# Performance work log

Measured on AMD Instinct MI355X. Metric: run time of the kernel, lower is better.

The kernel has to match this reference:

```python
import jax, jax.numpy as jnp
import numpy as np

B, T, E, H = 2, 2048, 1024, 16
HS = E // H  # head size = 64
EPS = 1e-5


def setup_inputs() -> dict:
    key = jax.random.key(0)
    ks = jax.random.split(key, 12)
    s_e = 1.0 / np.sqrt(E)
    s_4e = 1.0 / np.sqrt(4 * E)
    return {
        "x": jax.random.normal(ks[0], (B, T, E), dtype=jnp.float32),
        # per-head projections (no bias), stacked over heads: [H, E, HS]
        "Wq": jax.random.uniform(ks[1], (H, E, HS), jnp.float32, -s_e, s_e),
        "Wk": jax.random.uniform(ks[2], (H, E, HS), jnp.float32, -s_e, s_e),
        "Wv": jax.random.uniform(ks[3], (H, E, HS), jnp.float32, -s_e, s_e),
        # output projection
        "Wo": jax.random.uniform(ks[4], (E, E), jnp.float32, -s_e, s_e),
        "bo": jax.random.uniform(ks[5], (E,), jnp.float32, -s_e, s_e),
        # feed-forward
        "W1": jax.random.uniform(ks[6], (E, 4 * E), jnp.float32, -s_e, s_e),
        "b1": jax.random.uniform(ks[7], (4 * E,), jnp.float32, -s_e, s_e),
        "W2": jax.random.uniform(ks[8], (4 * E, E), jnp.float32, -s_4e, s_4e),
        "b2": jax.random.uniform(ks[9], (E,), jnp.float32, -s_4e, s_4e),
        # layernorms
        "g1": jnp.ones((E,), jnp.float32),
        "be1": jnp.zeros((E,), jnp.float32),
        "g2": jnp.ones((E,), jnp.float32),
        "be2": jnp.zeros((E,), jnp.float32),
    }


def _layernorm(x, g, b):
    mu = jnp.mean(x, axis=-1, keepdims=True)
    var = jnp.var(x, axis=-1, keepdims=True)
    return (x - mu) * jax.lax.rsqrt(var + EPS) * g + b


def reference(x, Wq, Wk, Wv, Wo, bo, W1, b1, W2, b2, g1, be1, g2, be2):
    Bx, Tx, Ex = x.shape
    # --- multi-head causal self-attention (dropout = identity in eval) ---
    q = jnp.einsum("bte,hed->bhtd", x, Wq)
    k = jnp.einsum("bte,hed->bhtd", x, Wk)
    v = jnp.einsum("bte,hed->bhtd", x, Wv)
    scale = HS ** -0.5
    scores = jnp.einsum("bhtd,bhsd->bhts", q, k) * scale  # [B,H,T,T]
    causal = jnp.tril(jnp.ones((Tx, Tx), dtype=bool))
    scores = jnp.where(causal, scores, -jnp.inf)
    att = jax.nn.softmax(scores, axis=-1)
    out = jnp.einsum("bhts,bhsd->bhtd", att, v)  # [B,H,T,HS]
    out = out.transpose(0, 2, 1, 3).reshape(Bx, Tx, Ex)  # concat heads
    out = out @ Wo + bo
    # --- residual + LN1 ---
    x = _layernorm(x + out, g1, be1)
    # --- feed-forward ---
    h = jax.nn.relu(x @ W1 + b1)
    ff = h @ W2 + b2
    # --- residual + LN2 ---
    return _layernorm(x + ff, g2, be2)
```

## Files before the change

### kernel.cpp

```cpp
#include <hip/hip_runtime.h>
#include <hip/hip_bf16.h>
#include <cstdint>
#include <cstddef>

typedef __hip_bfloat16 bf16;
typedef __attribute__((ext_vector_type(8))) short short8;
typedef __attribute__((ext_vector_type(4))) float f32x4;

#define B_  2
#define T_  2048
#define E_  1024
#define H_  16
#define HS_ 64
#define EPS_ 1e-5f
#define NEG_BIG -1.0e30f
#define SCL2E 0.18033688011112042f

__device__ __forceinline__ float b2f(bf16 v) { return __bfloat162float(v); }
__device__ __forceinline__ bf16  f2b(float v) { return __float2bfloat16(v); }
__device__ __forceinline__ ushort f2bs(float v) { bf16 b = __float2bfloat16(v); return *(ushort*)&b; }
__device__ __forceinline__ float ld1(const bf16* p) { return b2f(*p); }
__device__ __forceinline__ float ld1(const float* p) { return *p; }
__device__ __forceinline__ void st1(bf16* p, float v) { *p = f2b(v); }
__device__ __forceinline__ void st1(float* p, float v) { *p = v; }

__device__ __forceinline__ void ld4(const bf16* p, float v[4]) {
    ushort4 u = *(const ushort4*)p;
    v[0] = b2f(*(const bf16*)&u.x);
    v[1] = b2f(*(const bf16*)&u.y);
    v[2] = b2f(*(const bf16*)&u.z);
    v[3] = b2f(*(const bf16*)&u.w);
}
__device__ __forceinline__ void ld4(const float* p, float v[4]) {
    float4 f = *(const float4*)p;
    v[0] = f.x; v[1] = f.y; v[2] = f.z; v[3] = f.w;
}
__device__ __forceinline__ void st4(bf16* p, const float v[4]) {
    ushort4 u;
    u.x = f2bs(v[0]); u.y = f2bs(v[1]); u.z = f2bs(v[2]); u.w = f2bs(v[3]);
    *(ushort4*)p = u;
}
__device__ __forceinline__ void st4(float* p, const float v[4]) {
    float4 f; f.x = v[0]; f.y = v[1]; f.z = v[2]; f.w = v[3];
    *(float4*)p = f;
}

__device__ __forceinline__ float fexp2(float x) {
#if __has_builtin(__builtin_amdgcn_exp2f)
    return __builtin_amdgcn_exp2f(x);
#else
    return exp2f(x);
#endif
}

__device__ __forceinline__ void gload16(const void* g, const void* l) {
    __builtin_amdgcn_global_load_lds(
        (const __attribute__((address_space(1))) unsigned int*)(size_t)g,
        (__attribute__((address_space(3))) unsigned int*)(unsigned int)(size_t)l,
        16, 0, 0);
}

__device__ __forceinline__ void transpose_tile_s(short t[64][72],
                                                 const float* in, size_t ldin,
                                                 bf16* out, size_t ldout,
                                                 int r0, int c0)
{
    const int tid = threadIdx.x;
    const int tr = tid >> 2, tc4 = (tid & 3) * 16;

    const float* p = in + (size_t)(r0 + tr) * ldin + c0 + tc4;
    float4 v0 = ((const float4*)p)[0], v1 = ((const float4*)p)[1];
    float4 v2 = ((const float4*)p)[2], v3 = ((const float4*)p)[3];
    union { ushort u[16]; uint4 q[2]; } pk;
    pk.u[0] = f2bs(v0.x); pk.u[1] = f2bs(v0.y); pk.u[2]  = f2bs(v0.z); pk.u[3]  = f2bs(v0.w);
    pk.u[4] = f2bs(v1.x); pk.u[5] = f2bs(v1.y); pk.u[6]  = f2bs(v1.z); pk.u[7]  = f2bs(v1.w);
    pk.u[8] = f2bs(v2.x); pk.u[9] = f2bs(v2.y); pk.u[10] = f2bs(v2.z); pk.u[11] = f2bs(v2.w);
    pk.u[12] = f2bs(v3.x); pk.u[13] = f2bs(v3.y); pk.u[14] = f2bs(v3.z); pk.u[15] = f2bs(v3.w);
    *(uint4*)&t[tr][tc4]     = pk.q[0];
    *(uint4*)&t[tr][tc4 + 8] = pk.q[1];
    __syncthreads();

    const int tcI = tid >> 2, rj = (tid & 3) * 16;
    union { ushort u[16]; uint4 q[2]; } po;
    #pragma unroll
    for (int j = 0; j < 16; j++) po.u[j] = (ushort)t[rj + j][tcI];
    bf16* op = out + (size_t)(c0 + tcI) * ldout + r0 + rj;
    ((uint4*)op)[0] = po.q[0];
    ((uint4*)op)[1] = po.q[1];
}

__global__ __launch_bounds__(256) void prep_kernel(const float* __restrict__ x,
                                                   ushort* __restrict__ xb,
                                                   const float* __restrict__ Wq,
                                                   const float* __restrict__ Wk,
                                                   const float* __restrict__ Wv,
                                                   bf16* __restrict__ WqkvT,
                                                   const float* __restrict__ Wo,
                                                   bf16* __restrict__ WoT)
{
    __shared__ short t[64][72];
    const int bid = blockIdx.x;
    if (bid < 2048) {
        int i = (bid * 256 + (int)threadIdx.x) * 8;
        float4 a = ((const float4*)(x + i))[0];
        float4 b = ((const float4*)(x + i))[1];
        union { ushort u[8]; uint4 v; } p;
        p.u[0] = f2bs(a.x); p.u[1] = f2bs(a.y); p.u[2] = f2bs(a.z); p.u[3] = f2bs(a.w);
        p.u[4] = f2bs(b.x); p.u[5] = f2bs(b.y); p.u[6] = f2bs(b.z); p.u[7] = f2bs(b.w);
        *(uint4*)(xb + i) = p.v;
    } else if (bid < 2048 + 768) {
        const int i = bid - 2048;
        const int s = i >> 4, xt = i & 15;
        const int proj = s >> 4, h = s & 15;
        const float* W = (proj == 0) ? Wq : ((proj == 1) ? Wk : Wv);
        transpose_tile_s(t, W + (size_t)h * E_ * HS_, HS_,
                         WqkvT + ((size_t)proj * E_ + h * 64) * E_, E_,
                         xt * 64, 0);
    } else {
        const int i = bid - 2816;
        transpose_tile_s(t, Wo, E_, WoT, E_, (i >> 4) * 64, (i & 15) * 64);
    }
}

__global__ __launch_bounds__(256) void prep2_kernel(const float* __restrict__ W1,
                                                    bf16* __restrict__ W1T,
                                                    const float* __restrict__ W2,
                                                    bf16* __restrict__ W2T)
{
    __shared__ short t[64][72];
    const int bid = blockIdx.x;
    if (bid < 1024) {
        transpose_tile_s(t, W1, 4 * E_, W1T, E_,
                         (bid & 15) * 64, (bid >> 4) * 64);
    } else {
        const int i = bid - 1024;
        transpose_tile_s(t, W2, E_, W2T, 4 * E_,
                         (i >> 4) * 64, (i & 15) * 64);
    }
}

template <int WROWS, int WCOLS, int MF, int NF, int KS, bool BIAS, bool RELU,
          bool ACC, bool VSPLIT, typename TO>
__global__ __launch_bounds__(256) void gemm_bt(const bf16* __restrict__ A,
                                               const bf16* __restrict__ BT,
                                               const float* __restrict__ bias,
                                               TO* __restrict__ C,
                                               bf16* __restrict__ vTout,
                                               int M, int N, int K, int ldb)
{
    constexpr int BM = WROWS * MF * 16;
    constexpr int BN = WCOLS * NF * 16;
    __shared__ short Asm[KS][BM][32];
    __shared__ short Bsm[KS][BN][32];

    const int tid  = threadIdx.x;
    const int wv   = tid >> 6, lane = tid & 63;
    const int quad = lane >> 4, l16 = lane & 15;

    const int gx = gridDim.x;
    const int p  = blockIdx.y * gx + blockIdx.x;
    const int spx = gx >> 3;
    const int xcd = p & 7, j = p >> 3;
    const int bx = xcd * spx + (j % spx);
    const int by = j / spx;

    const int row0 = by * BM, col0 = bx * BN;
    const int mr0  = (wv / WCOLS) * MF * 16;
    const int nc0  = (wv % WCOLS) * NF * 16;

    const int sr = tid >> 2, sc = tid & 3;
    const bf16* Ag = A  + (size_t)(row0 + sr) * K + sc * 8;
    const bf16* Bg = BT + (size_t)(col0 + (sr % BN)) * ldb + sc * 8;

    f32x4 acc[MF][NF];
    #pragma unroll
    for (int i = 0; i < MF; i++)
        #pragma unroll
        for (int j2 = 0; j2 < NF; j2++) acc[i][j2] = (f32x4){0.f, 0.f, 0.f, 0.f};

    for (int kt = 0; kt < K; kt += 32 * KS) {
        __syncthreads();
        #pragma unroll
        for (int g = 0; g < KS; g++) {
            #pragma unroll
            for (int l = 0; l < BM / 64; l++)
                gload16(Ag + g * 32 + (size_t)l * 64 * K, &Asm[g][l * 64 + wv * 16][0]);
            #pragma unroll
            for (int l = 0; l < BN / 64; l++)
                gload16(Bg + g * 32 + (size_t)l * 64 * ldb, &Bsm[g][l * 64 + wv * 16][0]);
        }
        Ag += 32 * KS; Bg += 32 * KS;
        __syncthreads();

        #pragma unroll
        for (int g = 0; g < KS; g++) {
            short8 af[MF], bfr[NF];
            #pragma unroll
            for (int mf = 0; mf < MF; mf++)
                af[mf] = *(const short8*)&Asm[g][mr0 + mf * 16 + l16][quad * 8];
            #pragma unroll
            for (int nf = 0; nf < NF; nf++)
                bfr[nf] = *(const short8*)&Bsm[g][nc0 + nf * 16 + l16][quad * 8];
            #pragma unroll
            for (int mf = 0; mf < MF; mf++)
                #pragma unroll
                for (int nf = 0; nf < NF; nf++)
                    acc[mf][nf] = __builtin_amdgcn_mfma_f32_16x16x32_bf16(
                        af[mf], bfr[nf], acc[mf][nf], 0, 0, 0);
        }
    }

    if (VSPLIT && col0 >= 2 * E_) {
        #pragma unroll
        for (int nf = 0; nf < NF; nf++) {
            const int cv = col0 + nc0 + nf * 16 + l16 - 2 * E_;
            const int hh = cv >> 6, dd = cv & 63;
            #pragma unroll
            for (int mf = 0; mf < MF; mf++) {
                const int row = row0 + mr0 + mf * 16 + quad * 4;
                const int bb = row >> 11, tt = row & (T_ - 1);
                ushort4 u;
                u.x = f2bs(acc[mf][nf][0]);
                u.y = f2bs(acc[mf][nf][1]);
                u.z = f2bs(acc[mf][nf][2]);
                u.w = f2bs(acc[mf][nf][3]);
                *(ushort4*)(vTout + ((size_t)(bb * H_ + hh) * 64 + dd) * T_ + tt) = u;
            }
        }
    } else {
        #pragma unroll
        for (int nf = 0; nf < NF; nf++) {
            const int col = col0 + nc0 + nf * 16 + l16;
            const float bv = BIAS ? bias[col] : 0.f;
            #pragma unroll
            for (int mf = 0; mf < MF; mf++) {
                #pragma unroll
                for (int r = 0; r < 4; r++) {
                    const int row = row0 + mr0 + mf * 16 + quad * 4 + r;
                    float v = acc[mf][nf][r] + bv;
                    if (ACC) v += ld1(&C[(size_t)row * N + col]);
                    if (RELU) v = fmaxf(v, 0.f);
                    st1(&C[(size_t)row * N + col], v);
                }
            }
        }
    }
}

__global__ __launch_bounds__(256) void attn_mfma(const bf16* __restrict__ qkv,
                                                 const bf16* __restrict__ vT,
                                                 bf16* __restrict__ outp)
{
    __shared__ short Klds[128][72];
    __shared__ short Vlds[64][136];
    __shared__ short Plds[4][16][136];

    const int tid  = threadIdx.x;
    const int w    = tid >> 6, lane = tid & 63;
    const int quad = lane >> 4, l16 = lane & 15;

    const int p    = blockIdx.y * 32 + blockIdx.x;
    const int bh   = (p & 7) * 4 + ((p >> 3) & 3);
    const int tile = 31 - (p >> 5);
    const int b    = bh >> 4, h = bh & 15;
    const size_t rowb = (size_t)b * T_ * 3 * E_;
    const int t0    = tile * 64;
    const int qbase = t0 + w * 16;

    const int kkey = tid >> 1, kdh = (tid & 1) * 32;
    const bf16* Kg = qkv + rowb + E_ + h * HS_ + kdh;
    const int vd = tid >> 2, vseg = (tid & 3) * 32;
    const bf16* Vg = vT + ((size_t)bh * 64 + vd) * T_ + vseg;

    short8 vone;
    #pragma unroll
    for (int j = 0; j < 8; j++) vone[j] = (short)0x3F80;

    const bf16* Qp = qkv + rowb + (size_t)(qbase + l16) * (3 * E_) + h * HS_;
    const short8 aq0 = *(const short8*)(Qp + quad * 8);
    const short8 aq1 = *(const short8*)(Qp + 32 + quad * 8);

    f32x4 o[4], o4;
    #pragma unroll
    for (int f = 0; f < 4; f++) o[f] = (f32x4){0.f, 0.f, 0.f, 0.f};
    o4 = (f32x4){0.f, 0.f, 0.f, 0.f};
    float mrow = NEG_BIG;

    for (int kt0 = 0; kt0 <= t0; kt0 += 128) {
        __syncthreads();
        {
            const int kr = (kt0 + kkey < T_) ? kt0 + kkey : T_ - 1;
            const bf16* kp = Kg + (size_t)kr * (3 * E_);
            *(uint4*)&Klds[kkey][kdh]      = ((const uint4*)kp)[0];
            *(uint4*)&Klds[kkey][kdh + 8]  = ((const uint4*)kp)[1];
            *(uint4*)&Klds[kkey][kdh + 16] = ((const uint4*)kp)[2];
            *(uint4*)&Klds[kkey][kdh + 24] = ((const uint4*)kp)[3];
            const bf16* vp = Vg + kt0;
            *(uint4*)&Vlds[vd][vseg]       = ((const uint4*)vp)[0];
            *(uint4*)&Vlds[vd][vseg + 8]   = ((const uint4*)vp)[1];
            *(uint4*)&Vlds[vd][vseg + 16]  = ((const uint4*)vp)[2];
            *(uint4*)&Vlds[vd][vseg + 24]  = ((const uint4*)vp)[3];
        }
        __syncthreads();

        const bool active = (kt0 <= qbase + 15);
        const int nv0 = ((qbase + 15 - kt0) >> 4) + 1;
        const int nvalid = active ? (nv0 < 8 ? nv0 : 8) : 0;

        float ps[8][4];
        #pragma unroll
        for (int c = 0; c < 8; c++) {
            if (c < nvalid) {
                const int kc = kt0 + c * 16;
                const int krow = c * 16 + l16;
                short8 bk0 = *(const short8*)&Klds[krow][quad * 8];
                short8 bk1 = *(const short8*)&Klds[krow][32 + quad * 8];
                f32x4 s = (f32x4){0.f, 0.f, 0.f, 0.f};
                s = __builtin_amdgcn_mfma_f32_16x16x32_bf16(bk0, aq0, s, 0, 0, 0);
                s = __builtin_amdgcn_mfma_f32_16x16x32_bf16(bk1, aq1, s, 0, 0, 0);
                const bool needmask = (kc + 15 > qbase);
                #pragma unroll
                for (int r = 0; r < 4; r++) {
                    float sv = s[r] * SCL2E;
                    if (needmask && (kc + quad * 4 + r > qbase + l16)) sv = NEG_BIG;
                    ps[c][r] = sv;
                }
            }
        }
        if (active) {
            float mx = ps[0][0];
            #pragma unroll
            for (int r = 1; r < 4; r++) mx = fmaxf(mx, ps[0][r]);
            #pragma unroll
            for (int c = 1; c < 8; c++)
                if (c < nvalid)
                    #pragma unroll
                    for (int r = 0; r < 4; r++) mx = fmaxf(mx, ps[c][r]);
            mx = fmaxf(mx, __shfl_xor(mx, 16));
            mx = fmaxf(mx, __shfl_xor(mx, 32));
            const float mnew = fmaxf(mrow, mx);
            const float al = fexp2(mrow - mnew);
            mrow = mnew;

            #pragma unroll
            for (int c = 0; c < 8; c++) {
                uint2 pk; pk.x = 0u; pk.y = 0u;
                if (c < nvalid) {
                    const float e0 = fexp2(ps[c][0] - mnew);
                    const float e1 = fexp2(ps[c][1] - mnew);
                    const float e2 = fexp2(ps[c][2] - mnew);
                    const float e3 = fexp2(ps[c][3] - mnew);
                    pk.x = (uint)f2bs(e0) | ((uint)f2bs(e1) << 16);
                    pk.y = (uint)f2bs(e2) | ((uint)f2bs(e3) << 16);
                }
                *(uint2*)&Plds[w][l16][c * 16 + quad * 4] = pk;
            }

            float alo[4];
            #pragma unroll
            for (int r = 0; r < 4; r++) alo[r] = __shfl(al, quad * 4 + r);
            #pragma unroll
            for (int f = 0; f < 4; f++)
                #pragma unroll
                for (int r = 0; r < 4; r++) o[f][r] *= alo[r];
            #pragma unroll
            for (int r = 0; r < 4; r++) o4[r] *= alo[r];

            #pragma unroll
            for (int kg = 0; kg < 4; kg++) {
                short8 pa = *(const short8*)&Plds[w][l16][kg * 32 + quad * 8];
                #pragma unroll
                for (int f = 0; f < 4; f++) {
                    short8 vb = *(const short8*)&Vlds[f * 16 + l16][kg * 32 + quad * 8];
                    o[f] = __builtin_amdgcn_mfma_f32_16x16x32_bf16(pa, vb, o[f], 0, 0, 0);
                }
                o4 = __builtin_amdgcn_mfma_f32_16x16x32_bf16(pa, vone, o4, 0, 0, 0);
            }
        }
    }

    #pragma unroll
    for (int r = 0; r < 4; r++) {
        const float linv = 1.f / o4[r];
        bf16* op = outp + (size_t)(b * T_ + qbase + quad * 4 + r) * E_ + h * HS_;
        #pragma unroll
        for (int f = 0; f < 4; f++)
            op[f * 16 + l16] = f2b(o[f][r] * linv);
    }
}

template <typename TA, typename TR, typename TO>
__global__ __launch_bounds__(256) void ln_kernel(const TA* a,
                                                 const TR* r,
                                                 const float* g,
                                                 const float* be,
                                                 TO* out)
{
    const int row = blockIdx.x;
    const int c0  = (int)threadIdx.x * 4;
    const TA* pa = a + (size_t)row * E_ + c0;
    const TR* pr = r + (size_t)row * E_ + c0;
    TO* po = out + (size_t)row * E_ + c0;

    float va[4], vr[4], v[4];
    ld4(pa, va);
    ld4(pr, vr);
    float sum = 0.f, sq = 0.f;
    #pragma unroll
    for (int j = 0; j < 4; j++) {
        v[j] = va[j] + vr[j];
        sum += v[j];
        sq  += v[j] * v[j];
    }
    #pragma unroll
    for (int o = 32; o >= 1; o >>= 1) {
        sum += __shfl_xor(sum, o);
        sq  += __shfl_xor(sq, o);
    }
    __shared__ float red[8];
    const int wave = threadIdx.x >> 6, lane = threadIdx.x & 63;
    if (lane == 0) { red[wave] = sum; red[4 + wave] = sq; }
    __syncthreads();
    sum = red[0] + red[1] + red[2] + red[3];
    sq  = red[4] + red[5] + red[6] + red[7];

    const float mu  = sum * (1.f / E_);
    const float var = fmaxf(sq * (1.f / E_) - mu * mu, 0.f);
    const float rs  = rsqrtf(var + EPS_);

    const float4 gv = *(const float4*)(g + c0);
    const float4 bv = *(const float4*)(be + c0);
    float ov[4];
    ov[0] = (v[0] - mu) * rs * gv.x + bv.x;
    ov[1] = (v[1] - mu) * rs * gv.y + bv.y;
    ov[2] = (v[2] - mu) * rs * gv.z + bv.z;
    ov[3] = (v[3] - mu) * rs * gv.w + bv.w;
    st4(po, ov);
}

extern "C" void kernel_launch(void* const* d_in, const int* in_sizes, int n_in,
                              void* d_out, int out_size, void* d_ws, size_t ws_size,
                              hipStream_t stream)
{
    (void)in_sizes; (void)n_in; (void)out_size; (void)ws_size;
    const float* x   = (const float*)d_in[0];
    const float* Wq  = (const float*)d_in[1];
    const float* Wk  = (const float*)d_in[2];
    const float* Wv  = (const float*)d_in[3];
    const float* Wo  = (const float*)d_in[4];
    const float* bo  = (const float*)d_in[5];
    const float* W1  = (const float*)d_in[6];
    const float* b1  = (const float*)d_in[7];
    const float* W2  = (const float*)d_in[8];
    const float* b2  = (const float*)d_in[9];
    const float* g1  = (const float*)d_in[10];
    const float* be1 = (const float*)d_in[11];
    const float* g2  = (const float*)d_in[12];
    const float* be2 = (const float*)d_in[13];

    const int M = B_ * T_;
    char* ws = (char*)d_ws;
    bf16* WqkvT = (bf16*)(ws);
    bf16* qkv   = (bf16*)(ws + (size_t)6291456);
    bf16* WoT   = (bf16*)(ws + (size_t)31457280);
    bf16* W1T   = (bf16*)(ws);
    bf16* W2T   = (bf16*)(ws + (size_t)8388608);
    bf16* proj  = (bf16*)(ws + (size_t)16777216);
    bf16* y     = (bf16*)(ws + (size_t)25165824);
    bf16* ff    = (bf16*)(ws + (size_t)16777216);

    bf16*  xb      = (bf16*)d_out;
    bf16*  vT      = (bf16*)((char*)d_out + (size_t)8388608);
    bf16*  attnout = (bf16*)d_out;
    bf16*  hbuf    = (bf16*)d_out;
    float* outf    = (float*)d_out;

    prep_kernel<<<3072, 256, 0, stream>>>(x, (ushort*)xb, Wq, Wk, Wv, WqkvT, Wo, WoT);

    gemm_bt<2, 2, 4, 4, 2, false, false, false, true, bf16><<<dim3(24, 32), 256, 0, stream>>>(
        xb, WqkvT, nullptr, qkv, vT, M, 3 * E_, E_, E_);

    attn_mfma<<<dim3(32, 32), 256, 0, stream>>>(qkv, vT, attnout);

    prep2_kernel<<<2048, 256, 0, stream>>>(W1, W1T, W2, W2T);

    gemm_bt<2, 2, 4, 2, 4, true, false, false, false, bf16><<<dim3(16, 32), 256, 0, stream>>>(
        attnout, WoT, bo, proj, nullptr, M, E_, E_, E_);

    ln_kernel<float, bf16, bf16><<<M, 256, 0, stream>>>(x, proj, g1, be1, y);

    for (int half = 0; half < 2; half++) {
        const size_t c0 = (size_t)half * 2048;
        gemm_bt<2, 2, 4, 4, 4, true, true, false, false, bf16><<<dim3(16, 32), 256, 0, stream>>>(
            y, W1T + c0 * E_, b1 + c0, hbuf, nullptr, M, 2048, E_, E_);
        if (half == 0)
            gemm_bt<2, 2, 4, 2, 4, true, false, false, false, bf16><<<dim3(16, 32), 256, 0, stream>>>(
                hbuf, W2T + c0, b2, ff, nullptr, M, E_, 2048, 4 * E_);
        else
            gemm_bt<2, 2, 4, 2, 4, false, false, true, false, bf16><<<dim3(16, 32), 256, 0, stream>>>(
                hbuf, W2T + c0, nullptr, ff, nullptr, M, E_, 2048, 4 * E_);
    }

    ln_kernel<bf16, bf16, float><<<M, 256, 0, stream>>>(y, ff, g2, be2, outf);
}
```

Baseline: 365.7 us.

## Double-buffer LDS tiles in GEMM to overlap global loads with MFMA

Adds a DBUF template option that splits shared memory into two buffers. The kernel now issues global-to-LDS loads for the next K tile while MFMAs run on the current one, and needs only one barrier per tile. It is enabled for the Wo and FFN GEMMs, with KS halved from 4 to 2 so the LDS footprint stays about the same. The aim is to hide global load latency behind compute, though the smaller KS means more loop iterations.

```diff
diff --git a/kernel.cpp b/kernel.cpp
--- a/kernel.cpp
+++ b/kernel.cpp
@@ -139,8 +139,8 @@
     }
 }
 
-template <int WROWS, int WCOLS, int MF, int NF, int KS, bool BIAS, bool RELU,
-          bool ACC, bool VSPLIT, typename TO>
+template <int WROWS, int WCOLS, int MF, int NF, int KS, bool DBUF, bool BIAS,
+          bool RELU, bool ACC, bool VSPLIT, typename TO>
 __global__ __launch_bounds__(256) void gemm_bt(const bf16* __restrict__ A,
                                                const bf16* __restrict__ BT,
                                                const float* __restrict__ bias,
@@ -150,8 +150,9 @@
 {
     constexpr int BM = WROWS * MF * 16;
     constexpr int BN = WCOLS * NF * 16;
-    __shared__ short Asm[KS][BM][32];
-    __shared__ short Bsm[KS][BN][32];
+    constexpr int NB = DBUF ? 2 : 1;
+    __shared__ short Asm[NB][KS][BM][32];
+    __shared__ short Bsm[NB][KS][BN][32];
 
     const int tid  = threadIdx.x;
     const int wv   = tid >> 6, lane = tid & 63;
@@ -178,35 +179,54 @@
         #pragma unroll
         for (int j2 = 0; j2 < NF; j2++) acc[i][j2] = (f32x4){0.f, 0.f, 0.f, 0.f};
 
-    for (int kt = 0; kt < K; kt += 32 * KS) {
-        __syncthreads();
+    auto stage = [&](int nb) {
         #pragma unroll
         for (int g = 0; g < KS; g++) {
             #pragma unroll
             for (int l = 0; l < BM / 64; l++)
-                gload16(Ag + g * 32 + (size_t)l * 64 * K, &Asm[g][l * 64 + wv * 16][0]);
+                gload16(Ag + g * 32 + (size_t)l * 64 * K, &Asm[nb][g][l * 64 + wv * 16][0]);
             #pragma unroll
             for (int l = 0; l < BN / 64; l++)
-                gload16(Bg + g * 32 + (size_t)l * 64 * ldb, &Bsm[g][l * 64 + wv * 16][0]);
+                gload16(Bg + g * 32 + (size_t)l * 64 * ldb, &Bsm[nb][g][l * 64 + wv * 16][0]);
         }
         Ag += 32 * KS; Bg += 32 * KS;
-        __syncthreads();
-
+    };
+    auto compute = [&](int nb) {
         #pragma unroll
         for (int g = 0; g < KS; g++) {
             short8 af[MF], bfr[NF];
             #pragma unroll
             for (int mf = 0; mf < MF; mf++)
-                af[mf] = *(const short8*)&Asm[g][mr0 + mf * 16 + l16][quad * 8];
+                af[mf] = *(const short8*)&Asm[nb][g][mr0 + mf * 16 + l16][quad * 8];
             #pragma unroll
             for (int nf = 0; nf < NF; nf++)
-                bfr[nf] = *(const short8*)&Bsm[g][nc0 + nf * 16 + l16][quad * 8];
+                bfr[nf] = *(const short8*)&Bsm[nb][g][nc0 + nf * 16 + l16][quad * 8];
             #pragma unroll
             for (int mf = 0; mf < MF; mf++)
                 #pragma unroll
                 for (int nf = 0; nf < NF; nf++)
                     acc[mf][nf] = __builtin_amdgcn_mfma_f32_16x16x32_bf16(
                         af[mf], bfr[nf], acc[mf][nf], 0, 0, 0);
+        }
+    };
+
+    if (DBUF) {
+        const int nt = K / (32 * KS);
+        stage(0);
+        for (int t = 0; t < nt; t += 2) {
+            __syncthreads();
+            if (t + 1 < nt) stage(1);
+            compute(0);
+            __syncthreads();
+            if (t + 2 < nt) stage(0);
+            compute(1);
+        }
+    } else {
+        for (int kt = 0; kt < K; kt += 32 * KS) {
+            __syncthreads();
+            stage(0);
+            __syncthreads();
+            compute(0);
         }
     }
 
@@ -477,27 +497,27 @@
 
     prep_kernel<<<3072, 256, 0, stream>>>(x, (ushort*)xb, Wq, Wk, Wv, WqkvT, Wo, WoT);
 
-    gemm_bt<2, 2, 4, 4, 2, false, false, false, true, bf16><<<dim3(24, 32), 256, 0, stream>>>(
+    gemm_bt<2, 2, 4, 4, 2, false, false, false, false, true, bf16><<<dim3(24, 32), 256, 0, stream>>>(
         xb, WqkvT, nullptr, qkv, vT, M, 3 * E_, E_, E_);
 
     attn_mfma<<<dim3(32, 32), 256, 0, stream>>>(qkv, vT, attnout);
 
     prep2_kernel<<<2048, 256, 0, stream>>>(W1, W1T, W2, W2T);
 
-    gemm_bt<2, 2, 4, 2, 4, true, false, false, false, bf16><<<dim3(16, 32), 256, 0, stream>>>(
+    gemm_bt<2, 2, 4, 2, 2, true, true, false, false, false, bf16><<<dim3(16, 32), 256, 0, stream>>>(
         attnout, WoT, bo, proj, nullptr, M, E_, E_, E_);
 
     ln_kernel<float, bf16, bf16><<<M, 256, 0, stream>>>(x, proj, g1, be1, y);
 
     for (int half = 0; half < 2; half++) {
         const size_t c0 = (size_t)half * 2048;
-        gemm_bt<2, 2, 4, 4, 4, true, true, false, false, bf16><<<dim3(16, 32), 256, 0, stream>>>(
+        gemm_bt<2, 2, 4, 4, 2, true, true, true, false, false, bf16><<<dim3(16, 32), 256, 0, stream>>>(
             y, W1T + c0 * E_, b1 + c0, hbuf, nullptr, M, 2048, E_, E_);
         if (half == 0)
-            gemm_bt<2, 2, 4, 2, 4, true, false, false, false, bf16><<<dim3(16, 32), 256, 0, stream>>>(
+            gemm_bt<2, 2, 4, 2, 2, true, true, false, false, false, bf16><<<dim3(16, 32), 256, 0, stream>>>(
                 hbuf, W2T + c0, b2, ff, nullptr, M, E_, 2048, 4 * E_);
         else
-            gemm_bt<2, 2, 4, 2, 4, false, false, true, false, bf16><<<dim3(16, 32), 256, 0, stream>>>(
+            gemm_bt<2, 2, 4, 2, 2, true, false, false, true, false, bf16><<<dim3(16, 32), 256, 0, stream>>>(
                 hbuf, W2T + c0, nullptr, ff, nullptr, M, E_, 2048, 4 * E_);
     }
 
```

Result: faster. 357.4 us (-2.3%).
